# Performance work log

Hardware: AMD Instinct MI355X
Metric: run time of the kernel (lower is better)

## Reference

```python
import jax, jax.numpy as jnp
import numpy as np

N_HEADS = 16
D_HEAD = 64
D_MODEL = 1024


def setup_inputs() -> dict:
    key = jax.random.key(0)
    k_x, k_q, k_k, k_v, k_o = jax.random.split(key, 5)
    std = 1.0 / np.sqrt(D_MODEL)
    B, T = 4, 2048
    return {
        "x": jax.random.normal(k_x, (B, T, D_MODEL), dtype=jnp.float32),
        "W_Q": jax.random.normal(k_q, (D_MODEL, N_HEADS * D_HEAD), dtype=jnp.float32) * std,
        "W_K": jax.random.normal(k_k, (D_MODEL, N_HEADS * D_HEAD), dtype=jnp.float32) * std,
        "W_V": jax.random.normal(k_v, (D_MODEL, N_HEADS * D_HEAD), dtype=jnp.float32) * std,
        "W_O": jax.random.normal(k_o, (N_HEADS * D_HEAD, D_MODEL), dtype=jnp.float32) * std,
    }


def reference(x, W_Q, W_K, W_V, W_O):
    B, T, _ = x.shape
    H, D = N_HEADS, D_HEAD
    # projections: [B,T,H,D]
    q = (x @ W_Q).reshape(B, T, H, D)
    k = (x @ W_K).reshape(B, T, H, D)
    v = (x @ W_V).reshape(B, T, H, D)
    scale = 1.0 / jnp.sqrt(jnp.asarray(D, dtype=x.dtype))
    # scores: [B,H,T,T]
    scores = jnp.einsum("bqhd,bkhd->bhqk", q, k) * scale
    causal = jnp.tril(jnp.ones((T, T), dtype=bool))
    scores = jnp.where(causal[None, None], scores, jnp.asarray(-jnp.inf, dtype=scores.dtype))
    attn = jax.nn.softmax(scores, axis=-1)
    out = jnp.einsum("bhqk,bkhd->bqhd", attn, v).reshape(B, T, H * D)
    return out @ W_O
```

## Files before the change

kernel.cpp:

```cpp
#include <hip/hip_runtime.h>

typedef unsigned short u16;
typedef short bf16x8 __attribute__((ext_vector_type(8)));
typedef float f32x4 __attribute__((ext_vector_type(4)));

__device__ inline u16 f32_to_bf16(float f) {
  union { float f; unsigned int u; } v; v.f = f;
  unsigned int r = v.u + 0x7FFFu + ((v.u >> 16) & 1u);
  return (u16)(r >> 16);
}

__device__ inline float red16_sum(float x) {
#pragma unroll
  for (int m = 8; m >= 1; m >>= 1) x += __shfl_xor(x, m);
  return x;
}

__device__ __forceinline__ void gl_lds16(const u16* g, u16* l) {
  __builtin_amdgcn_global_load_lds(
      (const __attribute__((address_space(1))) void*)g,
      (__attribute__((address_space(3))) void*)l, 16, 0, 0);
}

__global__ __launch_bounds__(256) void xcvt_kernel(const float* __restrict__ in,
                                                   u16* __restrict__ out) {
  size_t i = (size_t)blockIdx.x * 256 + threadIdx.x;
  float4 f0 = ((const float4*)in)[2 * i];
  float4 f1 = ((const float4*)in)[2 * i + 1];
  union { u16 t[8]; uint4 v; } pk;
  pk.t[0] = f32_to_bf16(f0.x); pk.t[1] = f32_to_bf16(f0.y);
  pk.t[2] = f32_to_bf16(f0.z); pk.t[3] = f32_to_bf16(f0.w);
  pk.t[4] = f32_to_bf16(f1.x); pk.t[5] = f32_to_bf16(f1.y);
  pk.t[6] = f32_to_bf16(f1.z); pk.t[7] = f32_to_bf16(f1.w);
  ((uint4*)out)[i] = pk.v;
}

__global__ __launch_bounds__(256) void transpose_cvt4_kernel(const float* __restrict__ i0,
                                                             const float* __restrict__ i1,
                                                             const float* __restrict__ i2,
                                                             const float* __restrict__ i3,
                                                             u16* __restrict__ wbase) {
  const int z = blockIdx.z;
  const float* in = (z == 0) ? i0 : (z == 1) ? i1 : (z == 2) ? i2 : i3;
  u16* out = wbase + (size_t)z * (1 << 20);
  __shared__ __align__(16) float tile[32][33];
  const int tx = threadIdx.x & 31, ty = threadIdx.x >> 5;
  const int bx = blockIdx.x * 32, by = blockIdx.y * 32;
#pragma unroll
  for (int i = 0; i < 32; i += 8)
    tile[ty + i][tx] = in[(size_t)(by + ty + i) * 1024 + bx + tx];
  __syncthreads();
#pragma unroll
  for (int i = 0; i < 32; i += 8)
    out[(size_t)(bx + ty + i) * 1024 + by + tx] = f32_to_bf16(tile[tx][ty + i]);
}

__global__ __launch_bounds__(256) void gemm_qkv_kernel(const u16* __restrict__ A,
                                                       const u16* __restrict__ Bt,
                                                       u16* __restrict__ Q,
                                                       u16* __restrict__ K,
                                                       u16* __restrict__ Vt) {
  __shared__ u16 sA[128 * 64];
  __shared__ u16 sB[128 * 64];

  const int tid = threadIdx.x;
  const int lane = tid & 63, wave = tid >> 6;
  const int quad = lane >> 4, l16 = lane & 15;
  const int bn = blockIdx.x, bm = blockIdx.y;
  const int m0 = bm * 128, n0 = bn * 128;
  const int wm = (wave >> 1) * 64, wn = (wave & 1) * 64;

  const int lr = lane >> 3;
  const int gsw = (lane & 7) ^ (lr & 7);
  const int sw0 = ((0 * 4 + quad) ^ (l16 & 7)) * 8;
  const int sw1 = ((1 * 4 + quad) ^ (l16 & 7)) * 8;

  f32x4 acc[4][4] = {};

  for (int k0 = 0; k0 < 1024; k0 += 64) {
    __syncthreads();
#pragma unroll
    for (int i = 0; i < 4; ++i) {
      int c = wave * 4 + i;
      int row = c * 8 + lr;
      gl_lds16(A + (size_t)(m0 + row) * 1024 + k0 + gsw * 8, sA + c * 512);
      gl_lds16(Bt + (size_t)(n0 + row) * 1024 + k0 + gsw * 8, sB + c * 512);
    }
    __syncthreads();

#pragma unroll
    for (int kk = 0; kk < 2; ++kk) {
      const int sw = kk ? sw1 : sw0;
      bf16x8 afr[4], bfr[4];
#pragma unroll
      for (int mt = 0; mt < 4; ++mt)
        afr[mt] = *(const bf16x8*)(sA + (wm + mt * 16 + l16) * 64 + sw);
#pragma unroll
      for (int nt = 0; nt < 4; ++nt)
        bfr[nt] = *(const bf16x8*)(sB + (wn + nt * 16 + l16) * 64 + sw);
#pragma unroll
      for (int mt = 0; mt < 4; ++mt)
#pragma unroll
        for (int nt = 0; nt < 4; ++nt)
          acc[mt][nt] = __builtin_amdgcn_mfma_f32_16x16x32_bf16(afr[mt], bfr[nt],
                                                                acc[mt][nt], 0, 0, 0);
    }
  }

  const int proj = bn >> 3;
#pragma unroll
  for (int mt = 0; mt < 4; ++mt) {
#pragma unroll
    for (int nt = 0; nt < 4; ++nt) {
#pragma unroll
      for (int r = 0; r < 4; ++r) {
        int mrow = m0 + wm + mt * 16 + quad * 4 + r;
        int nloc = (n0 & 1023) + wn + nt * 16 + l16;
        u16 bv = f32_to_bf16(acc[mt][nt][r]);
        if (proj == 0) {
          Q[(size_t)mrow * 1024 + nloc] = bv;
        } else if (proj == 1) {
          K[(size_t)mrow * 1024 + nloc] = bv;
        } else {
          int b = mrow >> 11, t = mrow & 2047;
          int h = nloc >> 6, d = nloc & 63;
          Vt[((size_t)((b * 16 + h) * 64 + d)) * 2048 + t] = bv;
        }
      }
    }
  }
}

__global__ __launch_bounds__(256) void gemm_out_kernel(const u16* __restrict__ A,
                                                       const u16* __restrict__ Bt,
                                                       float* __restrict__ C) {
  __shared__ u16 sA[128 * 64];
  __shared__ u16 sB[128 * 64];

  const int tid = threadIdx.x;
  const int lane = tid & 63, wave = tid >> 6;
  const int quad = lane >> 4, l16 = lane & 15;
  const int bn = blockIdx.x, bm = blockIdx.y;
  const int m0 = bm * 128, n0 = bn * 128;
  const int wm = (wave >> 1) * 64, wn = (wave & 1) * 64;

  const int lr = lane >> 3;
  const int gsw = (lane & 7) ^ (lr & 7);
  const int sw0 = ((0 * 4 + quad) ^ (l16 & 7)) * 8;
  const int sw1 = ((1 * 4 + quad) ^ (l16 & 7)) * 8;

  f32x4 acc[4][4] = {};

  for (int k0 = 0; k0 < 1024; k0 += 64) {
    __syncthreads();
#pragma unroll
    for (int i = 0; i < 4; ++i) {
      int c = wave * 4 + i;
      int row = c * 8 + lr;
      gl_lds16(A + (size_t)(m0 + row) * 1024 + k0 + gsw * 8, sA + c * 512);
      gl_lds16(Bt + (size_t)(n0 + row) * 1024 + k0 + gsw * 8, sB + c * 512);
    }
    __syncthreads();

#pragma unroll
    for (int kk = 0; kk < 2; ++kk) {
      const int sw = kk ? sw1 : sw0;
      bf16x8 afr[4], bfr[4];
#pragma unroll
      for (int mt = 0; mt < 4; ++mt)
        afr[mt] = *(const bf16x8*)(sA + (wm + mt * 16 + l16) * 64 + sw);
#pragma unroll
      for (int nt = 0; nt < 4; ++nt)
        bfr[nt] = *(const bf16x8*)(sB + (wn + nt * 16 + l16) * 64 + sw);
#pragma unroll
      for (int mt = 0; mt < 4; ++mt)
#pragma unroll
        for (int nt = 0; nt < 4; ++nt)
          acc[mt][nt] = __builtin_amdgcn_mfma_f32_16x16x32_bf16(afr[mt], bfr[nt],
                                                                acc[mt][nt], 0, 0, 0);
    }
  }

#pragma unroll
  for (int mt = 0; mt < 4; ++mt)
#pragma unroll
    for (int nt = 0; nt < 4; ++nt)
#pragma unroll
      for (int r = 0; r < 4; ++r) {
        int mrow = m0 + wm + mt * 16 + quad * 4 + r;
        int ncol = n0 + wn + nt * 16 + l16;
        C[(size_t)mrow * 1024 + ncol] = acc[mt][nt][r];
      }
}

#define LDS_S 72

__global__ __launch_bounds__(256, 4) void attn_kernel(const u16* __restrict__ Qm,
                                                      const u16* __restrict__ Km,
                                                      const u16* __restrict__ Vt,
                                                      u16* __restrict__ Ctx) {
  const int pi = blockIdx.x;
  const int h = blockIdx.y, b = blockIdx.z;
  const int tid = threadIdx.x, lane = tid & 63, wave = tid >> 6;
  const int quad = lane >> 4, l16 = lane & 15;
  const int q64[2] = {pi, 31 - pi};

  __shared__ __align__(16) u16 sK[64 * LDS_S];
  __shared__ __align__(16) u16 sV[64 * LDS_S];
  __shared__ __align__(16) u16 sP[4][2][16 * LDS_S];

  bf16x8 qf[2][2];
#pragma unroll
  for (int s = 0; s < 2; ++s) {
    const size_t qrow = (size_t)(b * 2048 + q64[s] * 64 + wave * 16 + l16);
#pragma unroll
    for (int kk = 0; kk < 2; ++kk)
      qf[s][kk] = *(const bf16x8*)(Qm + qrow * 1024 + h * 64 + kk * 32 + quad * 8);
  }

  f32x4 o_acc[2][4] = {};
  float ps[2][4] = {};

  const int nkt = 32 - pi;
  for (int kt = 0; kt < nkt; ++kt) {
    const int k0 = kt * 64;
    __syncthreads();
#pragma unroll
    for (int i = 0; i < 2; ++i) {
      int c = tid + 256 * i;
      int row = c >> 3, col = (c & 7) * 8;
      *(uint4*)(sK + row * LDS_S + col) =
          *(const uint4*)(Km + ((size_t)(b * 2048 + k0 + row)) * 1024 + h * 64 + col);
      *(uint4*)(sV + row * LDS_S + col) =
          *(const uint4*)(Vt + ((size_t)((b * 16 + h) * 64 + row)) * 2048 + k0 + col);
    }
    __syncthreads();

#pragma unroll
    for (int s = 0; s < 2; ++s) {
      const int qmin = q64[s] * 64 + wave * 16;
      if (k0 > qmin + 15) continue;

      f32x4 sc[4];
#pragma unroll
      for (int nt = 0; nt < 4; ++nt) {
        f32x4 a = {};
#pragma unroll
        for (int kk = 0; kk < 2; ++kk) {
          bf16x8 kf = *(const bf16x8*)(sK + (nt * 16 + l16) * LDS_S + kk * 32 + quad * 8);
          a = __builtin_amdgcn_mfma_f32_16x16x32_bf16(qf[s][kk], kf, a, 0, 0, 0);
        }
        sc[nt] = a;
      }

      const bool need_mask = (k0 + 63) > qmin;
#pragma unroll
      for (int nt = 0; nt < 4; ++nt) {
#pragma unroll
        for (int r = 0; r < 4; ++r) {
          float v = sc[nt][r] * 0.125f;
          if (need_mask) {
            int qi = qmin + quad * 4 + r;
            int kj = k0 + nt * 16 + l16;
            if (kj > qi) v = -1e30f;
          }
          float p = __expf(v);
          sc[nt][r] = p;
          ps[s][r] += p;
        }
      }

#pragma unroll
      for (int nt = 0; nt < 4; ++nt)
#pragma unroll
        for (int r = 0; r < 4; ++r)
          sP[wave][s][(quad * 4 + r) * LDS_S + nt * 16 + l16] = f32_to_bf16(sc[nt][r]);

#pragma unroll
      for (int kk = 0; kk < 2; ++kk) {
        bf16x8 pf = *(const bf16x8*)(sP[wave][s] + l16 * LDS_S + kk * 32 + quad * 8);
#pragma unroll
        for (int dt = 0; dt < 4; ++dt) {
          bf16x8 vf = *(const bf16x8*)(sV + (dt * 16 + l16) * LDS_S + kk * 32 + quad * 8);
          o_acc[s][dt] = __builtin_amdgcn_mfma_f32_16x16x32_bf16(pf, vf,
                                                                 o_acc[s][dt], 0, 0, 0);
        }
      }
    }
  }

  float inv_l[2][4];
#pragma unroll
  for (int s = 0; s < 2; ++s)
#pragma unroll
    for (int r = 0; r < 4; ++r)
      inv_l[s][r] = 1.0f / red16_sum(ps[s][r]);

#pragma unroll
  for (int s = 0; s < 2; ++s)
#pragma unroll
    for (int dt = 0; dt < 4; ++dt)
#pragma unroll
      for (int r = 0; r < 4; ++r) {
        int trow = q64[s] * 64 + wave * 16 + quad * 4 + r;
        Ctx[((size_t)(b * 2048 + trow)) * 1024 + h * 64 + dt * 16 + l16] =
            f32_to_bf16(o_acc[s][dt][r] * inv_l[s][r]);
      }
}

extern "C" void kernel_launch(void* const* d_in, const int* in_sizes, int n_in,
                              void* d_out, int out_size, void* d_ws, size_t ws_size,
                              hipStream_t stream) {
  const float* x  = (const float*)d_in[0];
  const float* wq = (const float*)d_in[1];
  const float* wk = (const float*)d_in[2];
  const float* wv = (const float*)d_in[3];
  const float* wo = (const float*)d_in[4];
  u16* ws = (u16*)d_ws;

  u16* wtqkv = ws;
  u16* wto  = ws + 3 * (size_t)(1 << 20);
  u16* Q    = ws + 4 * (size_t)(1 << 20);
  u16* K    = ws + 12 * (size_t)(1 << 20);
  u16* Vt   = ws + 20 * (size_t)(1 << 20);
  u16* Ctx  = ws + 28 * (size_t)(1 << 20);
  u16* xb   = Ctx;
  float* out = (float*)d_out;

  dim3 tb(256);
  xcvt_kernel<<<dim3(4096), tb, 0, stream>>>(x, xb);
  transpose_cvt4_kernel<<<dim3(32, 32, 4), tb, 0, stream>>>(wq, wk, wv, wo, ws);

  gemm_qkv_kernel<<<dim3(24, 64), tb, 0, stream>>>(xb, wtqkv, Q, K, Vt);

  attn_kernel<<<dim3(16, 16, 4), tb, 0, stream>>>(Q, K, Vt, Ctx);

  gemm_out_kernel<<<dim3(8, 64), tb, 0, stream>>>(Ctx, wto, out);
}
```

Before: 292.3 us.

## Rewrite QKV GEMM as 256x256 double-buffered pipelined tile with block swizzle

The QKV projection GEMM moves from 128x128 tiles with 256 threads to 256x256 tiles with 512 threads (8 waves, 128x64 per wave). It double-buffers LDS in k-halves and prefetches the next k-tile with async global-to-LDS loads that are interleaved with the MFMA phases, using explicit vmcnt waits, barriers and setprio. The launch order is also swizzled for L2 locality. The intent is to hide global-load latency and raise arithmetic intensity per tile, at the cost of more registers and LDS, fewer blocks (384), and many barriers.

```diff
diff --git a/kernel.cpp b/kernel.cpp
--- a/kernel.cpp
+++ b/kernel.cpp
@@ -55,81 +55,139 @@
     out[(size_t)(bx + ty + i) * 1024 + by + tx] = f32_to_bf16(tile[tx][ty + i]);
 }
 
-__global__ __launch_bounds__(256) void gemm_qkv_kernel(const u16* __restrict__ A,
-                                                       const u16* __restrict__ Bt,
-                                                       u16* __restrict__ Q,
-                                                       u16* __restrict__ K,
-                                                       u16* __restrict__ Vt) {
-  __shared__ u16 sA[128 * 64];
-  __shared__ u16 sB[128 * 64];
+
+#define QKV_CFENCE asm volatile("" ::: "memory")
+#define QKV_BAR do { QKV_CFENCE; asm volatile("s_barrier" ::: "memory"); } while (0)
+#define QKV_VMW(n) asm volatile("s_waitcnt vmcnt(" #n ")" ::: "memory")
+#define QKV_LGK0 asm volatile("s_waitcnt lgkmcnt(0)" ::: "memory")
+
+#define STAGE_A(d2, kh, kt) do {                                   \
+    const u16* _p = A + aSrc + (size_t)(kt) * 64 + (kh) * 32;      \
+    gl_lds16(_p, &sA[d2][kh][dstOff]);                             \
+    gl_lds16(_p + 16 * 1024, &sA[d2][kh][dstOff + 512]);           \
+  } while (0)
+#define STAGE_B(d2, kh, kt) do {                                   \
+    const u16* _p = Bt + bSrc + (size_t)(kt) * 64 + (kh) * 32;     \
+    gl_lds16(_p, &sB[d2][kh][dstOff]);                             \
+    gl_lds16(_p + 16 * 1024, &sB[d2][kh][dstOff + 512]);           \
+  } while (0)
+#define LDA(d2, kk, mh) {                                          \
+    _Pragma("unroll") for (int mt = 0; mt < 4; ++mt)               \
+      afr[mt] = *(const bf16x8*)&sA[d2][kk][(mh) * 2048 + mt * 512 + aOff]; }
+#define LDB(d2, kk) {                                              \
+    _Pragma("unroll") for (int nt = 0; nt < 4; ++nt)               \
+      bfr[nt] = *(const bf16x8*)&sB[d2][kk][nt * 512 + bOff]; }
+#define MMA(mh) {                                                  \
+    _Pragma("unroll") for (int mt = 0; mt < 4; ++mt)               \
+      _Pragma("unroll") for (int nt = 0; nt < 4; ++nt)             \
+        acc[(mh) * 4 + mt][nt] = __builtin_amdgcn_mfma_f32_16x16x32_bf16( \
+            afr[mt], bfr[nt], acc[(mh) * 4 + mt][nt], 0, 0, 0); }
+
+__global__ __launch_bounds__(512, 2) void gemm_qkv_kernel(const u16* __restrict__ A,
+                                                          const u16* __restrict__ Bt,
+                                                          u16* __restrict__ Q,
+                                                          u16* __restrict__ K,
+                                                          u16* __restrict__ Vt) {
+  __shared__ __align__(16) u16 sA[2][2][256 * 32];
+  __shared__ __align__(16) u16 sB[2][2][256 * 32];
 
   const int tid = threadIdx.x;
   const int lane = tid & 63, wave = tid >> 6;
   const int quad = lane >> 4, l16 = lane & 15;
-  const int bn = blockIdx.x, bm = blockIdx.y;
-  const int m0 = bm * 128, n0 = bn * 128;
-  const int wm = (wave >> 1) * 64, wn = (wave & 1) * 64;
-
-  const int lr = lane >> 3;
-  const int gsw = (lane & 7) ^ (lr & 7);
-  const int sw0 = ((0 * 4 + quad) ^ (l16 & 7)) * 8;
-  const int sw1 = ((1 * 4 + quad) ^ (l16 & 7)) * 8;
-
-  f32x4 acc[4][4] = {};
-
-  for (int k0 = 0; k0 < 1024; k0 += 64) {
-    __syncthreads();
-#pragma unroll
-    for (int i = 0; i < 4; ++i) {
-      int c = wave * 4 + i;
-      int row = c * 8 + lr;
-      gl_lds16(A + (size_t)(m0 + row) * 1024 + k0 + gsw * 8, sA + c * 512);
-      gl_lds16(Bt + (size_t)(n0 + row) * 1024 + k0 + gsw * 8, sB + c * 512);
-    }
-    __syncthreads();
-
-#pragma unroll
-    for (int kk = 0; kk < 2; ++kk) {
-      const int sw = kk ? sw1 : sw0;
-      bf16x8 afr[4], bfr[4];
-#pragma unroll
-      for (int mt = 0; mt < 4; ++mt)
-        afr[mt] = *(const bf16x8*)(sA + (wm + mt * 16 + l16) * 64 + sw);
-#pragma unroll
-      for (int nt = 0; nt < 4; ++nt)
-        bfr[nt] = *(const bf16x8*)(sB + (wn + nt * 16 + l16) * 64 + sw);
-#pragma unroll
-      for (int mt = 0; mt < 4; ++mt)
-#pragma unroll
-        for (int nt = 0; nt < 4; ++nt)
-          acc[mt][nt] = __builtin_amdgcn_mfma_f32_16x16x32_bf16(afr[mt], bfr[nt],
-                                                                acc[mt][nt], 0, 0, 0);
-    }
-  }
-
-  const int proj = bn >> 3;
-#pragma unroll
-  for (int mt = 0; mt < 4; ++mt) {
+
+  const int lin = blockIdx.y * 12 + blockIdx.x;
+  const int swz = (lin & 7) * 48 + (lin >> 3);
+  const int bn = swz % 12, bm = swz / 12;
+  const int m0 = bm * 256, n0 = bn * 256;
+  const int wm = (wave >> 2) * 128, wn = (wave & 3) * 64;
+
+  const int sRow = lane >> 2;
+  const int sGrp = (lane & 3) ^ ((lane >> 3) & 3);
+  const size_t aSrc = (size_t)(m0 + wave * 32 + sRow) * 1024 + sGrp * 8;
+  const size_t bSrc = (size_t)(n0 + wave * 32 + sRow) * 1024 + sGrp * 8;
+  const int dstOff = wave * 1024;
+
+  const int swr = (quad ^ ((l16 >> 1) & 3)) * 8;
+  const int aOff = (wm + l16) * 32 + swr;
+  const int bOff = (wn + l16) * 32 + swr;
+
+  f32x4 acc[8][4] = {};
+  bf16x8 afr[4], bfr[4];
+
+  STAGE_A(0, 0, 0); STAGE_B(0, 0, 0); STAGE_A(0, 1, 0); STAGE_B(0, 1, 0);
+  QKV_VMW(4);
+  QKV_BAR;
+
+  for (int t = 0; t < 16; ++t) {
+    const int d = t & 1, dn = d ^ 1;
+    const bool pf = (t < 15);
+
+    LDA(d, 0, 0); LDB(d, 0);
+    if (pf) STAGE_A(dn, 0, t + 1);
+    QKV_BAR;
+    QKV_LGK0;
+    __builtin_amdgcn_s_setprio(1);
+    MMA(0);
+    __builtin_amdgcn_s_setprio(0);
+    QKV_BAR;
+
+    LDA(d, 0, 1);
+    if (pf) { STAGE_B(dn, 0, t + 1); QKV_VMW(4); } else { QKV_VMW(0); }
+    QKV_BAR;
+    QKV_LGK0;
+    __builtin_amdgcn_s_setprio(1);
+    MMA(1);
+    __builtin_amdgcn_s_setprio(0);
+    QKV_BAR;
+
+    LDA(d, 1, 0); LDB(d, 1);
+    if (pf) STAGE_A(dn, 1, t + 1);
+    QKV_BAR;
+    QKV_LGK0;
+    __builtin_amdgcn_s_setprio(1);
+    MMA(0);
+    __builtin_amdgcn_s_setprio(0);
+    QKV_BAR;
+
+    LDA(d, 1, 1);
+    if (pf) { STAGE_B(dn, 1, t + 1); QKV_VMW(4); }
+    QKV_BAR;
+    QKV_LGK0;
+    __builtin_amdgcn_s_setprio(1);
+    MMA(1);
+    __builtin_amdgcn_s_setprio(0);
+    QKV_BAR;
+  }
+
+  const int proj = bn >> 2;
+#pragma unroll
+  for (int mi = 0; mi < 8; ++mi) {
 #pragma unroll
     for (int nt = 0; nt < 4; ++nt) {
 #pragma unroll
       for (int r = 0; r < 4; ++r) {
-        int mrow = m0 + wm + mt * 16 + quad * 4 + r;
+        int mrow = m0 + wm + mi * 16 + quad * 4 + r;
         int nloc = (n0 & 1023) + wn + nt * 16 + l16;
-        u16 bv = f32_to_bf16(acc[mt][nt][r]);
+        u16 bv = f32_to_bf16(acc[mi][nt][r]);
         if (proj == 0) {
           Q[(size_t)mrow * 1024 + nloc] = bv;
         } else if (proj == 1) {
           K[(size_t)mrow * 1024 + nloc] = bv;
         } else {
-          int b = mrow >> 11, t = mrow & 2047;
-          int h = nloc >> 6, d = nloc & 63;
-          Vt[((size_t)((b * 16 + h) * 64 + d)) * 2048 + t] = bv;
+          int b = mrow >> 11, tt = mrow & 2047;
+          int h = nloc >> 6, dd = nloc & 63;
+          Vt[((size_t)((b * 16 + h) * 64 + dd)) * 2048 + tt] = bv;
         }
       }
     }
   }
 }
+
+#undef STAGE_A
+#undef STAGE_B
+#undef LDA
+#undef LDB
+#undef MMA
 
 __global__ __launch_bounds__(256) void gemm_out_kernel(const u16* __restrict__ A,
                                                        const u16* __restrict__ Bt,
@@ -331,7 +389,7 @@
   xcvt_kernel<<<dim3(4096), tb, 0, stream>>>(x, xb);
   transpose_cvt4_kernel<<<dim3(32, 32, 4), tb, 0, stream>>>(wq, wk, wv, wo, ws);
 
-  gemm_qkv_kernel<<<dim3(24, 64), tb, 0, stream>>>(xb, wtqkv, Q, K, Vt);
+  gemm_qkv_kernel<<<dim3(12, 32), dim3(512), 0, stream>>>(xb, wtqkv, Q, K, Vt);
 
   attn_kernel<<<dim3(16, 16, 4), tb, 0, stream>>>(Q, K, Vt, Ctx);
 
```

Measured after the change: 302.8 us. +3.6%, slower.
